# Kernel tuning notes

Measured on AMD Instinct MI355X. Metric: run time of the kernel, lower is better.

## Reference

```python
import jax, jax.numpy as jnp
import numpy as np

D_MODEL = 512
N = 2048
BS = 8


def setup_inputs() -> dict:
    key = jax.random.key(0)
    ks = jax.random.split(key, 5)
    inputs1 = jax.random.normal(ks[0], (BS, N, D_MODEL), dtype=jnp.float32)
    inputs2 = jax.random.normal(ks[1], (BS, N, D_MODEL), dtype=jnp.float32)
    # torch Linear weights: init.normal_(std=0.001), bias=0
    Wq = 0.001 * jax.random.normal(ks[2], (D_MODEL, D_MODEL), dtype=jnp.float32)
    Wk = 0.001 * jax.random.normal(ks[3], (D_MODEL, D_MODEL), dtype=jnp.float32)
    Wv = 0.001 * jax.random.normal(ks[4], (D_MODEL, D_MODEL), dtype=jnp.float32)
    bq = jnp.zeros((D_MODEL,), dtype=jnp.float32)
    bk = jnp.zeros((D_MODEL,), dtype=jnp.float32)
    bv = jnp.zeros((D_MODEL,), dtype=jnp.float32)
    # nn.Parameter(torch.ones((n, n)))
    position_biases = jnp.ones((N, N), dtype=jnp.float32)
    return {"inputs1": inputs1, "inputs2": inputs2, "Wq": Wq, "bq": bq,
            "Wk": Wk, "bk": bk, "Wv": Wv, "bv": bv,
            "position_biases": position_biases}


def reference(inputs1, inputs2, Wq, bq, Wk, bk, Wv, bv, position_biases):
    # torch Linear: y = x @ W.T + b
    q = inputs1 @ Wq.T + bq                     # [b, n, d]
    k = inputs1 @ Wk.T + bk                     # [b, s, d]
    v = inputs2 @ Wv.T + bv                     # [b, s, d]
    # exp(k[b,s,d] + bias[t,s]) = exp(bias)[t,s] * exp(k)[b,s,d] -> separable,
    # avoiding the original's (n, bs, n, dim) broadcast intermediate.
    expB = jnp.exp(position_biases)             # [t, s]
    ek = jnp.exp(k)                             # [b, s, d]
    num = jnp.einsum('ts,bsd->btd', expB, ek * v)
    den = jnp.einsum('ts,bsd->btd', expB, ek)
    return jax.nn.sigmoid(q) * (num / den)      # [b, n, d]
```

## Files before the change

kernel.cpp:

```cpp
#include <hip/hip_runtime.h>

typedef float  f32x4  __attribute__((ext_vector_type(4)));
typedef __bf16 bf16x8 __attribute__((ext_vector_type(8)));
typedef __bf16 bf16x4 __attribute__((ext_vector_type(4)));

#define D_MODEL 512
#define SEQ     2048
#define BATCH   8
#define ROWS    (BATCH * SEQ)

#define ASYNC_COPY16(dst_lds, src_glb)                                          \
  __builtin_amdgcn_global_load_lds(                                             \
      (const __attribute__((address_space(1))) void*)(src_glb),                 \
      (__attribute__((address_space(3))) void*)(dst_lds), 16, 0, 0)

__global__ void cvt_all_kernel(const float* __restrict__ x1,
                               const float* __restrict__ x2,
                               const float* __restrict__ posb,
                               const float* __restrict__ Wq,
                               const float* __restrict__ Wk,
                               const float* __restrict__ Wv,
                               __bf16* __restrict__ x1b, __bf16* __restrict__ x2b,
                               __bf16* __restrict__ expBb, __bf16* __restrict__ wb)
{
  const int blk = blockIdx.x;
  if (blk < 16384) {
    const float* in = (blk < 8192) ? x1 : x2;
    __bf16* out = (blk < 8192) ? x1b : x2b;
    const int i = (blk & 8191) * 256 + threadIdx.x;
    float4 v = ((const float4*)in)[i];
    bf16x4 o = { (__bf16)v.x, (__bf16)v.y, (__bf16)v.z, (__bf16)v.w };
    ((bf16x4*)out)[i] = o;
  } else if (blk < 20480) {
    const int i = (blk - 16384) * 256 + threadIdx.x;
    float4 v = ((const float4*)posb)[i];
    bf16x4 o = { (__bf16)__expf(v.x), (__bf16)__expf(v.y),
                 (__bf16)__expf(v.z), (__bf16)__expf(v.w) };
    ((bf16x4*)expBb)[i] = o;
  } else {
    const int i = (blk - 20480) * 256 + threadIdx.x;
    const int nW4 = D_MODEL * D_MODEL / 4;
    const float* src = (i < nW4) ? Wq : (i < 2 * nW4) ? Wk : Wv;
    const int ii = i - ((i < nW4) ? 0 : (i < 2 * nW4) ? nW4 : 2 * nW4);
    float4 v = ((const float4*)src)[ii];
    bf16x4 o = { (__bf16)v.x, (__bf16)v.y, (__bf16)v.z, (__bf16)v.w };
    ((bf16x4*)wb)[i] = o;
  }
}

__global__ __launch_bounds__(256) void tri_gemm_kernel(
    const __bf16* __restrict__ x1b, const __bf16* __restrict__ x2b,
    const __bf16* __restrict__ wb,
    const float* __restrict__ bq, const float* __restrict__ bk,
    const float* __restrict__ bv,
    __bf16* __restrict__ sigq, __bf16* __restrict__ kT,
    __bf16* __restrict__ vT)
{
  __shared__ __align__(16) __bf16 As[128 * 64];
  __shared__ __align__(16) __bf16 Bs[128 * 64];

  const int K = D_MODEL;
  const int z = blockIdx.z;
  const int tid  = threadIdx.x;
  const int wave = tid >> 6;
  const int lane = tid & 63;
  const int quad = lane >> 4;
  const int l16  = lane & 15;
  const int wm   = (wave >> 1) * 64;
  const int wn   = (wave & 1) * 64;
  const int l8r = lane >> 3;
  const int scol = ((lane & 7) ^ l8r) * 8;
  const int F0 = blockIdx.y * 128;

  const __bf16* Ap = (z == 0) ? x1b
                   : (z == 1) ? (wb + (long long)D_MODEL * D_MODEL)
                              : (wb + 2LL * D_MODEL * D_MODEL);
  const __bf16* Bp = (z == 0) ? wb : (z == 1) ? x1b : x2b;

  const int srow = wave * 8 + l8r;

  const __bf16* ga[4]; const __bf16* gb[4];
  auto set_tile = [&](int t) {
    const int L0 = (blockIdx.x * 2 + t) * 128;
    const int m0 = (z == 0) ? L0 : F0;
    const int n0 = (z == 0) ? F0 : L0;
    #pragma unroll
    for (int i = 0; i < 4; ++i) {
      ga[i] = Ap + (long long)(m0 + i * 32 + srow) * K + scol;
      gb[i] = Bp + (long long)(n0 + i * 32 + srow) * K + scol;
    }
  };
  auto stage = [&](int k0) {
    #pragma unroll
    for (int i = 0; i < 4; ++i) {
      ASYNC_COPY16(As + (i * 32 + wave * 8) * 64, ga[i] + k0);
      ASYNC_COPY16(Bs + (i * 32 + wave * 8) * 64, gb[i] + k0);
    }
  };

  set_tile(0);
  stage(0);

  for (int t = 0; t < 2; ++t) {
    f32x4 acc[4][4];
    #pragma unroll
    for (int i = 0; i < 4; ++i)
      #pragma unroll
      for (int j = 0; j < 4; ++j) acc[i][j] = (f32x4){0.f, 0.f, 0.f, 0.f};

    for (int k0 = 0; k0 < K; k0 += 64) {
      __syncthreads();
      #pragma unroll
      for (int kk = 0; kk < 2; ++kk) {
        const int slot = ((quad + kk * 4) ^ (l16 & 7)) * 8;
        bf16x8 af[4], bfr[4];
        #pragma unroll
        for (int i = 0; i < 4; ++i)
          af[i] = *(const bf16x8*)&As[(wm + i * 16 + l16) * 64 + slot];
        #pragma unroll
        for (int j = 0; j < 4; ++j)
          bfr[j] = *(const bf16x8*)&Bs[(wn + j * 16 + l16) * 64 + slot];
        #pragma unroll
        for (int i = 0; i < 4; ++i)
          #pragma unroll
          for (int j = 0; j < 4; ++j)
            acc[i][j] = __builtin_amdgcn_mfma_f32_16x16x32_bf16(af[i], bfr[j],
                                                                acc[i][j], 0, 0, 0);
      }
      __syncthreads();
      if (k0 + 64 < K) {
        stage(k0 + 64);
      } else if (t == 0) {
        set_tile(1);
        stage(0);
      }
    }

    const int L0 = (blockIdx.x * 2 + t) * 128;
    if (z == 0) {
      const int m0 = L0, n0 = F0;
      #pragma unroll
      for (int j = 0; j < 4; ++j) {
        const int col = n0 + wn + j * 16 + l16;
        const float bvv = bq[col];
        #pragma unroll
        for (int i = 0; i < 4; ++i)
          #pragma unroll
          for (int r = 0; r < 4; ++r) {
            const int row = m0 + wm + i * 16 + quad * 4 + r;
            float x = acc[i][j][r] + bvv;
            sigq[(long long)row * D_MODEL + col] =
                (__bf16)(1.f / (1.f + __expf(-x)));
          }
      }
    } else {
      const int m0 = F0, n0 = L0;
      const float* bias = (z == 1) ? bk : bv;
      __bf16* outp = (z == 1) ? kT : vT;
      #pragma unroll
      for (int i = 0; i < 4; ++i) {
        #pragma unroll
        for (int r = 0; r < 4; ++r) {
          const int d = m0 + wm + i * 16 + quad * 4 + r;
          const float bvv = bias[d];
          #pragma unroll
          for (int j = 0; j < 4; ++j) {
            const int rr = n0 + wn + j * 16 + l16;
            outp[(long long)d * ROWS + rr] = (__bf16)(acc[i][j][r] + bvv);
          }
        }
      }
    }
  }
}

__global__ __launch_bounds__(256) void combine_kernel(
    const __bf16* __restrict__ kT, const __bf16* __restrict__ vT,
    __bf16* __restrict__ ekvT)
{
  const int c = blockIdx.x * 256 + threadIdx.x;
  const int d   = c >> 11;
  const int off = (c & 2047) * 8;
  const int b = off >> 11;
  const int s = off & 2047;

  bf16x8 kk = *(const bf16x8*)(kT + (long long)d * ROWS + off);
  bf16x8 vv = *(const bf16x8*)(vT + (long long)d * ROWS + off);
  bf16x8 ek, ev;
  #pragma unroll
  for (int e = 0; e < 8; ++e) {
    float ekf = __expf((float)kk[e]);
    ek[e] = (__bf16)ekf;
    ev[e] = (__bf16)(ekf * (float)vv[e]);
  }
  const int gr = ((d >> 5) << 6) + (d & 31);
  __bf16* outp = ekvT + (long long)b * (2 * D_MODEL) * SEQ + s;
  *(bf16x8*)(outp + (long long)gr * SEQ)        = ev;
  *(bf16x8*)(outp + (long long)(gr + 32) * SEQ) = ek;
}

__global__ __launch_bounds__(256) void einsum_fused_kernel(
    const __bf16* __restrict__ A, const __bf16* __restrict__ BtAll,
    const __bf16* __restrict__ sigq, float* __restrict__ out)
{
  __shared__ __align__(16) __bf16 As[128 * 64];
  __shared__ __align__(16) __bf16 Bs[128 * 64];

  const int b = blockIdx.z;
  const __bf16* Bt = BtAll + (long long)b * (2 * D_MODEL) * SEQ;
  const int K = SEQ;

  const int tid  = threadIdx.x;
  const int wave = tid >> 6;
  const int lane = tid & 63;
  const int quad = lane >> 4;
  const int l16  = lane & 15;
  const int wm   = (wave >> 1) * 64;
  const int wn   = (wave & 1) * 64;
  const int m0 = blockIdx.x * 128;
  const int n0 = blockIdx.y * 128;
  const int l8r = lane >> 3;
  const int scol = ((lane & 7) ^ l8r) * 8;

  const __bf16* ga[4]; const __bf16* gb[4];
  __bf16* la[4]; __bf16* lb[4];
  #pragma unroll
  for (int i = 0; i < 4; ++i) {
    ga[i] = A  + (long long)(m0 + i * 32 + wave * 8 + l8r) * K + scol;
    gb[i] = Bt + (long long)(n0 + i * 32 + wave * 8 + l8r) * K + scol;
    la[i] = As + (i * 32 + wave * 8) * 64;
    lb[i] = Bs + (i * 32 + wave * 8) * 64;
  }

  f32x4 acc[4][4];
  #pragma unroll
  for (int i = 0; i < 4; ++i)
    #pragma unroll
    for (int j = 0; j < 4; ++j) acc[i][j] = (f32x4){0.f, 0.f, 0.f, 0.f};

  for (int k0 = 0; k0 < K; k0 += 64) {
    #pragma unroll
    for (int i = 0; i < 4; ++i) {
      ASYNC_COPY16(la[i], ga[i] + k0);
      ASYNC_COPY16(lb[i], gb[i] + k0);
    }
    __syncthreads();

    #pragma unroll
    for (int kk = 0; kk < 2; ++kk) {
      const int slot = ((quad + kk * 4) ^ (l16 & 7)) * 8;
      bf16x8 af[4], bfr[4];
      #pragma unroll
      for (int i = 0; i < 4; ++i)
        af[i] = *(const bf16x8*)&As[(wm + i * 16 + l16) * 64 + slot];
      #pragma unroll
      for (int j = 0; j < 4; ++j)
        bfr[j] = *(const bf16x8*)&Bs[(wn + j * 16 + l16) * 64 + slot];
      #pragma unroll
      for (int i = 0; i < 4; ++i)
        #pragma unroll
        for (int j = 0; j < 4; ++j)
          acc[i][j] = __builtin_amdgcn_mfma_f32_16x16x32_bf16(af[i], bfr[j],
                                                              acc[i][j], 0, 0, 0);
    }
    __syncthreads();
  }

  const int g = (n0 + wn) >> 6;
  #pragma unroll
  for (int j = 0; j < 2; ++j) {
    const int d = g * 32 + j * 16 + l16;
    #pragma unroll
    for (int i = 0; i < 4; ++i) {
      #pragma unroll
      for (int r = 0; r < 4; ++r) {
        const int row = m0 + wm + i * 16 + quad * 4 + r;
        const long long off = ((long long)b * SEQ + row) * D_MODEL + d;
        const float num = acc[i][j][r];
        const float den = acc[i][j + 2][r];
        out[off] = (float)sigq[off] * (num / den);
      }
    }
  }
}

extern "C" void kernel_launch(void* const* d_in, const int* in_sizes, int n_in,
                              void* d_out, int out_size, void* d_ws, size_t ws_size,
                              hipStream_t stream) {
  const float* inputs1 = (const float*)d_in[0];
  const float* inputs2 = (const float*)d_in[1];
  const float* Wq = (const float*)d_in[2];
  const float* bq = (const float*)d_in[3];
  const float* Wk = (const float*)d_in[4];
  const float* bk = (const float*)d_in[5];
  const float* Wv = (const float*)d_in[6];
  const float* bv = (const float*)d_in[7];
  const float* posb = (const float*)d_in[8];
  float* out = (float*)d_out;

  char* ws = (char*)d_ws;
  const long long szX  = (long long)ROWS * D_MODEL * 2;
  const long long szW  = (long long)D_MODEL * D_MODEL * 2;
  const long long szEB = (long long)SEQ * SEQ * 2;
  const long long szT  = (long long)BATCH * 2 * D_MODEL * SEQ * 2;
  __bf16* x1b   = (__bf16*)(ws);                 ws += szX;
  __bf16* x2b   = (__bf16*)(ws);                 ws += szX;
  __bf16* wb    = (__bf16*)(ws);                 ws += 3 * szW;
  __bf16* expBb = (__bf16*)(ws);                 ws += szEB;
  __bf16* sigq  = (__bf16*)(ws);                 ws += szX;
  __bf16* kT    = (__bf16*)(ws);                 ws += szX;
  __bf16* vT    = (__bf16*)(ws);                 ws += szX;
  __bf16* ekvT  = (__bf16*)(ws);                 ws += szT;

  cvt_all_kernel<<<21248, 256, 0, stream>>>(inputs1, inputs2, posb,
                                            Wq, Wk, Wv,
                                            x1b, x2b, expBb, wb);

  {
    dim3 g(ROWS / 256, D_MODEL / 128, 3);
    tri_gemm_kernel<<<g, 256, 0, stream>>>(x1b, x2b, wb, bq, bk, bv,
                                           sigq, kT, vT);
  }

  combine_kernel<<<(D_MODEL * ROWS / 8) / 256, 256, 0, stream>>>(kT, vT, ekvT);

  {
    dim3 g(SEQ / 128, (2 * D_MODEL) / 128, BATCH);
    einsum_fused_kernel<<<g, 256, 0, stream>>>(expBb, ekvT, sigq, out);
  }
}
```

Measured before the change: 265.4 us.

## Enlarge einsum tile to 256x256 with double-buffered async LDS pipeline

The einsum GEMM moves from 128x128 tiles with 256 threads to 256x256 tiles with 512 threads, backed by 128KB of dynamic shared memory. The next K-slice is loaded asynchronously into a second LDS buffer while the current one is computed, using explicit vmcnt waits, barriers and s_setprio around the MFMA bursts. The aim is more data reuse per block and global-load latency hidden behind compute. The cost is fewer blocks (256 in total), higher register pressure from 32 accumulators per thread, and extra barriers inside the inner loop.

```diff
diff --git a/kernel.cpp b/kernel.cpp
--- a/kernel.cpp
+++ b/kernel.cpp
@@ -199,71 +199,101 @@
   *(bf16x8*)(outp + (long long)(gr + 32) * SEQ) = ek;
 }
 
-__global__ __launch_bounds__(256) void einsum_fused_kernel(
+#define EBM 256
+#define EBN 256
+#define EBK 64
+#define ENT (SEQ / EBK)
+
+__global__ __launch_bounds__(512) void einsum_fused_kernel(
     const __bf16* __restrict__ A, const __bf16* __restrict__ BtAll,
     const __bf16* __restrict__ sigq, float* __restrict__ out)
 {
-  __shared__ __align__(16) __bf16 As[128 * 64];
-  __shared__ __align__(16) __bf16 Bs[128 * 64];
+  extern __shared__ __align__(16) __bf16 smem[];
 
   const int b = blockIdx.z;
   const __bf16* Bt = BtAll + (long long)b * (2 * D_MODEL) * SEQ;
-  const int K = SEQ;
 
   const int tid  = threadIdx.x;
   const int wave = tid >> 6;
   const int lane = tid & 63;
   const int quad = lane >> 4;
   const int l16  = lane & 15;
-  const int wm   = (wave >> 1) * 64;
-  const int wn   = (wave & 1) * 64;
-  const int m0 = blockIdx.x * 128;
-  const int n0 = blockIdx.y * 128;
-  const int l8r = lane >> 3;
+  const int wm   = (wave >> 2) * 128;
+  const int wn   = (wave & 3) * 64;
+  const int m0   = blockIdx.x * EBM;
+  const int n0   = blockIdx.y * EBN;
+  const int l8r  = lane >> 3;
   const int scol = ((lane & 7) ^ l8r) * 8;
 
-  const __bf16* ga[4]; const __bf16* gb[4];
-  __bf16* la[4]; __bf16* lb[4];
+  const __bf16* gA = A  + (long long)(m0 + wave * 8 + l8r) * SEQ + scol;
+  const __bf16* gB = Bt + (long long)(n0 + wave * 8 + l8r) * SEQ + scol;
+  __bf16* lA = smem +         (wave * 8) * 64;
+  __bf16* lB = smem + 32768 + (wave * 8) * 64;
+
+  f32x4 acc[8][4];
   #pragma unroll
-  for (int i = 0; i < 4; ++i) {
-    ga[i] = A  + (long long)(m0 + i * 32 + wave * 8 + l8r) * K + scol;
-    gb[i] = Bt + (long long)(n0 + i * 32 + wave * 8 + l8r) * K + scol;
-    la[i] = As + (i * 32 + wave * 8) * 64;
-    lb[i] = Bs + (i * 32 + wave * 8) * 64;
-  }
-
-  f32x4 acc[4][4];
-  #pragma unroll
-  for (int i = 0; i < 4; ++i)
+  for (int i = 0; i < 8; ++i)
     #pragma unroll
     for (int j = 0; j < 4; ++j) acc[i][j] = (f32x4){0.f, 0.f, 0.f, 0.f};
 
-  for (int k0 = 0; k0 < K; k0 += 64) {
+  auto stage = [&](int c, int k0) {
     #pragma unroll
     for (int i = 0; i < 4; ++i) {
-      ASYNC_COPY16(la[i], ga[i] + k0);
-      ASYNC_COPY16(lb[i], gb[i] + k0);
-    }
-    __syncthreads();
-
-    #pragma unroll
-    for (int kk = 0; kk < 2; ++kk) {
-      const int slot = ((quad + kk * 4) ^ (l16 & 7)) * 8;
-      bf16x8 af[4], bfr[4];
-      #pragma unroll
-      for (int i = 0; i < 4; ++i)
-        af[i] = *(const bf16x8*)&As[(wm + i * 16 + l16) * 64 + slot];
-      #pragma unroll
-      for (int j = 0; j < 4; ++j)
-        bfr[j] = *(const bf16x8*)&Bs[(wn + j * 16 + l16) * 64 + slot];
-      #pragma unroll
-      for (int i = 0; i < 4; ++i)
-        #pragma unroll
-        for (int j = 0; j < 4; ++j)
-          acc[i][j] = __builtin_amdgcn_mfma_f32_16x16x32_bf16(af[i], bfr[j],
-                                                              acc[i][j], 0, 0, 0);
-    }
-    __syncthreads();
+      ASYNC_COPY16(lA + c * 16384 + i * 4096, gA + (long long)i * 64 * SEQ + k0);
+      ASYNC_COPY16(lB + c * 16384 + i * 4096, gB + (long long)i * 64 * SEQ + k0);
+    }
+  };
+
+  stage(0, 0);
+
+  const int s0 = ((quad    ) ^ (l16 & 7)) * 8;
+  const int s1 = ((quad + 4) ^ (l16 & 7)) * 8;
+
+  for (int t = 0; t < ENT; ++t) {
+    const int c = t & 1;
+    if (t + 1 < ENT) {
+      stage(c ^ 1, (t + 1) * EBK);
+      asm volatile("s_waitcnt vmcnt(8)" ::: "memory");
+    } else {
+      asm volatile("s_waitcnt vmcnt(0)" ::: "memory");
+    }
+    __builtin_amdgcn_s_barrier();
+    __builtin_amdgcn_sched_barrier(0);
+
+    const __bf16* Ac = smem +         c * 16384 + (wm + l16) * 64;
+    const __bf16* Bc = smem + 32768 + c * 16384 + (wn + l16) * 64;
+
+    bf16x8 bfr[4][2];
+    #pragma unroll
+    for (int q = 0; q < 4; ++q) {
+      if (q == 0) {
+        #pragma unroll
+        for (int j = 0; j < 4; ++j) {
+          bfr[j][0] = *(const bf16x8*)&Bc[j * 1024 + s0];
+          bfr[j][1] = *(const bf16x8*)&Bc[j * 1024 + s1];
+        }
+      }
+      bf16x8 af[2][2];
+      #pragma unroll
+      for (int ii = 0; ii < 2; ++ii) {
+        af[ii][0] = *(const bf16x8*)&Ac[(q * 2 + ii) * 1024 + s0];
+        af[ii][1] = *(const bf16x8*)&Ac[(q * 2 + ii) * 1024 + s1];
+      }
+      __builtin_amdgcn_s_barrier();
+      asm volatile("s_waitcnt lgkmcnt(0)" ::: "memory");
+      __builtin_amdgcn_sched_barrier(0);
+      __builtin_amdgcn_s_setprio(1);
+      #pragma unroll
+      for (int kk = 0; kk < 2; ++kk)
+        #pragma unroll
+        for (int ii = 0; ii < 2; ++ii)
+          #pragma unroll
+          for (int j = 0; j < 4; ++j)
+            acc[q * 2 + ii][j] = __builtin_amdgcn_mfma_f32_16x16x32_bf16(
+                af[ii][kk], bfr[j][kk], acc[q * 2 + ii][j], 0, 0, 0);
+      __builtin_amdgcn_s_setprio(0);
+      __builtin_amdgcn_s_barrier();
+    }
   }
 
   const int g = (n0 + wn) >> 6;
@@ -271,7 +301,7 @@
   for (int j = 0; j < 2; ++j) {
     const int d = g * 32 + j * 16 + l16;
     #pragma unroll
-    for (int i = 0; i < 4; ++i) {
+    for (int i = 0; i < 8; ++i) {
       #pragma unroll
       for (int r = 0; r < 4; ++r) {
         const int row = m0 + wm + i * 16 + quad * 4 + r;
@@ -312,6 +342,13 @@
   __bf16* vT    = (__bf16*)(ws);                 ws += szX;
   __bf16* ekvT  = (__bf16*)(ws);                 ws += szT;
 
+  static bool attr_done = false;
+  if (!attr_done) {
+    hipFuncSetAttribute((const void*)einsum_fused_kernel,
+                        hipFuncAttributeMaxDynamicSharedMemorySize, 131072);
+    attr_done = true;
+  }
+
   cvt_all_kernel<<<21248, 256, 0, stream>>>(inputs1, inputs2, posb,
                                             Wq, Wk, Wv,
                                             x1b, x2b, expBb, wb);
@@ -325,7 +362,7 @@
   combine_kernel<<<(D_MODEL * ROWS / 8) / 256, 256, 0, stream>>>(kT, vT, ekvT);
 
   {
-    dim3 g(SEQ / 128, (2 * D_MODEL) / 128, BATCH);
-    einsum_fused_kernel<<<g, 256, 0, stream>>>(expBb, ekvT, sigq, out);
-  }
-}
+    dim3 g(SEQ / EBM, (2 * D_MODEL) / EBN, BATCH);
+    einsum_fused_kernel<<<g, 512, 131072, stream>>>(expBb, ekvT, sigq, out);
+  }
+}
```

Result: no change. 261.8 us (-1.3%).
